# Performance work log

Measured on AMD Instinct MI355X. Metric: run time of the kernel, lower is better.

The kernel has to match this reference:

```python
import jax, jax.numpy as jnp
import numpy as np

LAMBDA = 10.0      # sinkhorn_lambda from init_kwargs
N_ITERS = 100      # fixed Sinkhorn iteration count
B, T_MAX, D_MAX = 256, 256, 256
TP, DP = T_MAX + 1, D_MAX + 1   # expanded with births/deaths row+col
L = TP * DP                      # padded flat output length per example
EPS = 1e-12


def setup_inputs() -> dict:
    key = jax.random.key(0)
    k1, k2, k3 = jax.random.split(key, 3)
    affinity_scores = jax.random.uniform(k1, (B, T_MAX, D_MAX), dtype=jnp.float32)
    num_detections = jax.random.randint(k2, (B,), 32, D_MAX + 1, dtype=jnp.int32)
    num_tracklets = jax.random.randint(k3, (B,), 32, T_MAX + 1, dtype=jnp.int32)
    return {
        "affinity_scores": affinity_scores,
        "num_detections": num_detections,
        "num_tracklets": num_tracklets,
    }


def _sinkhorn_transport(aff, nd, nt):
    """Masked Sinkhorn on the expanded (nt+1)x(nd+1) matrix, padded to [TP,DP]."""
    r = jnp.arange(TP)
    c = jnp.arange(DP)
    row_valid = r <= nt          # nt tracklet rows + 1 births/deaths row
    col_valid = c <= nd
    interior = (r[:, None] < nt) & (c[None, :] < nd)
    aff_pad = jnp.pad(aff, ((0, 1), (0, 1)))
    aff_e = jnp.where(interior, aff_pad, 0.0)   # dummy row/col have affinity 0
    mask = (row_valid[:, None] & col_valid[None, :]).astype(aff.dtype)
    # cost = -affinity  =>  kernel K = exp(-lambda * cost) = exp(lambda * affinity)
    K = jnp.exp(LAMBDA * aff_e) * mask
    ndf = nd.astype(aff.dtype)
    ntf = nt.astype(aff.dtype)
    # target marginals: [1,...,1, length] on valid entries, 0 on padding
    row_sums = jnp.where(r < nt, 1.0, jnp.where(r == nt, ndf, 0.0))
    col_sums = jnp.where(c < nd, 1.0, jnp.where(c == nd, ntf, 0.0))
    u0 = jnp.zeros((TP,), aff.dtype)
    v0 = col_valid.astype(aff.dtype)

    def body(carry, _):
        u, v = carry
        u = jnp.where(row_valid, row_sums / (K @ v + EPS), 0.0)
        v = jnp.where(col_valid, col_sums / (K.T @ u + EPS), 0.0)
        return (u, v), None

    (u, v), _ = jax.lax.scan(body, (u0, v0), None, length=N_ITERS)
    transport = u[:, None] * K * v[None, :]
    return transport, interior, row_valid, col_valid


def _single(aff, nd, nt):
    transport, interior, row_valid, col_valid = _sinkhorn_transport(aff, nd, nt)
    r = jnp.arange(TP)
    c = jnp.arange(DP)

    # hard assignment on transport[:-1,:-1] (valid interior): mutual argmax
    neg_inf = jnp.array(-jnp.inf, transport.dtype)
    t_in = jnp.where(interior, transport, neg_inf)
    row_max = jnp.max(t_in, axis=1, keepdims=True)
    col_max = jnp.max(t_in, axis=0, keepdims=True)
    assign_in = interior & (t_in == row_max) & (t_in == col_max)
    # births/deaths: unmatched tracklets -> death col nd; unmatched detections -> birth row nt
    row_has = jnp.any(assign_in, axis=1)
    col_has = jnp.any(assign_in, axis=0)
    deaths = (r[:, None] < nt) & (c[None, :] == nd) & (~row_has)[:, None]
    births = (r[:, None] == nt) & (c[None, :] < nd) & (~col_has)[None, :]
    assignment = assign_in | deaths | births

    # flatten the (nt+1)x(nd+1) valid submatrix row-major, zero-pad to length L
    k = jnp.arange(L)
    length = (nt + 1) * (nd + 1)
    rr = jnp.clip(k // (nd + 1), 0, T_MAX)
    cc = k % (nd + 1)
    valid = k < length
    t_flat = jnp.where(valid, transport[rr, cc], 0.0)
    a_flat = jnp.where(valid, assignment[rr, cc], False)
    return t_flat, a_flat


def reference(affinity_scores, num_detections, num_tracklets):
    t_flat, a_flat = jax.vmap(_single)(affinity_scores, num_detections, num_tracklets)
    return t_flat, a_flat
```

## Files before the change

kernel.cpp:

```cpp
#include <hip/hip_runtime.h>


#define T_MAX   256
#define L_FLAT  (257 * 257)
#define N_ITERS 100
#define LAMBDA_F 10.0f
#define EPS_F    1e-12f
#define RS      260

#define QX1  0xB1
#define QX2  0x4E
#define ROR4 0x124
#define ROR8 0x128

template<int CTRL>
__device__ __forceinline__ float dpp_addf(float x) {
    int t = __builtin_amdgcn_update_dpp(0, __float_as_int(x), CTRL, 0xF, 0xF, true);
    return x + __int_as_float(t);
}
template<int CTRL>
__device__ __forceinline__ float dpp_maxf(float x) {
    int t = __builtin_amdgcn_update_dpp(0, __float_as_int(x), CTRL, 0xF, 0xF, true);
    return fmaxf(x, __int_as_float(t));
}
template<int CTRL>
__device__ __forceinline__ int dpp_ori(int x) {
    int t = __builtin_amdgcn_update_dpp(0, x, CTRL, 0xF, 0xF, true);
    return x | t;
}
__device__ __forceinline__ float swz16_addf(float x) {
    return x + __int_as_float(__builtin_amdgcn_ds_swizzle(__float_as_int(x), 0x401F));
}
__device__ __forceinline__ float swz16_maxf(float x) {
    return fmaxf(x, __int_as_float(__builtin_amdgcn_ds_swizzle(__float_as_int(x), 0x401F)));
}
__device__ __forceinline__ int swz16_ori(int x) {
    return x | __builtin_amdgcn_ds_swizzle(x, 0x401F);
}
__device__ __forceinline__ float fast_rcp(float x) {
#if __has_builtin(__builtin_amdgcn_rcpf)
    return __builtin_amdgcn_rcpf(x);
#else
    return 1.0f / x;
#endif
}
__device__ __forceinline__ float sel4(float a, float b, float c, float d, int rg) {
    float lo = (rg & 1) ? b : a;
    float hi = (rg & 1) ? d : c;
    return (rg & 2) ? hi : lo;
}

__global__ __launch_bounds__(512, 2) void assoc_sinkhorn_kernel(
    const float* __restrict__ aff,
    const int*   __restrict__ ndet,
    const int*   __restrict__ ntrk,
    float*       __restrict__ out_t,
    float*       __restrict__ out_a)
{
    const int b   = blockIdx.x;
    const int nd  = ndet[b];
    const int nt  = ntrk[b];
    const int tid = threadIdx.x;
    const int w   = tid >> 6;
    const int l   = tid & 63;
    const int rg  = l & 3;
    const int cg  = l >> 2;
    const int R0  = (w << 5) + (rg << 3);
    const int C0  = cg << 4;

    __shared__ __align__(16) float red[8 * RS];
    __shared__ __align__(16) float varr[256];
    __shared__ __align__(16) float cmax_s[256];
    __shared__ __align__(16) float supart[8];
    __shared__ __align__(16) float svpart[2][8];

    const float ndf = (float)nd;
    const float ntf = (float)nt;

    float K[8][16];
    {
        const float* Ab = aff + (size_t)b * (T_MAX * T_MAX);
        #pragma unroll
        for (int i = 0; i < 8; ++i) {
            const int r = R0 + i;
            const bool rv = (r < nt);
            const float* row = Ab + (size_t)r * T_MAX + C0;
            #pragma unroll
            for (int k = 0; k < 4; ++k) {
                const float4 x = *reinterpret_cast<const float4*>(row + 4 * k);
                const float a4[4] = {x.x, x.y, x.z, x.w};
                #pragma unroll
                for (int e = 0; e < 4; ++e) {
                    const int j = 4 * k + e;
                    K[i][j] = (rv && (C0 + j) < nd) ? expf(LAMBDA_F * a4[e]) : 0.0f;
                }
            }
        }
    }

    if (tid < 256) varr[tid] = (tid < nd) ? 1.0f : 0.0f;
    if (tid < 8)   svpart[0][tid] = (tid == 0) ? ndf : 0.0f;
    __syncthreads();

    float u[8];
    #pragma unroll
    for (int i = 0; i < 8; ++i) u[i] = 0.f;
    float vbd = 1.0f;
    float ubd = 0.0f;

    const int s2c   = tid >> 1;
    const int s2sub = tid & 1;

    for (int it = 0; it < N_ITERS; ++it) {
        float v[16];
        {
            const float4 a0 = *reinterpret_cast<const float4*>(&varr[C0]);
            const float4 a1 = *reinterpret_cast<const float4*>(&varr[C0 + 4]);
            const float4 a2 = *reinterpret_cast<const float4*>(&varr[C0 + 8]);
            const float4 a3 = *reinterpret_cast<const float4*>(&varr[C0 + 12]);
            v[0]=a0.x; v[1]=a0.y; v[2]=a0.z; v[3]=a0.w;
            v[4]=a1.x; v[5]=a1.y; v[6]=a1.z; v[7]=a1.w;
            v[8]=a2.x; v[9]=a2.y; v[10]=a2.z; v[11]=a2.w;
            v[12]=a3.x; v[13]=a3.y; v[14]=a3.z; v[15]=a3.w;
        }
        float p[8];
        #pragma unroll
        for (int i = 0; i < 8; ++i) {
            float s = 0.f;
            #pragma unroll
            for (int j = 0; j < 16; ++j) s = fmaf(K[i][j], v[j], s);
            p[i] = s;
        }
        #pragma unroll
        for (int i = 0; i < 8; ++i) p[i] = dpp_addf<ROR4>(p[i]);
        #pragma unroll
        for (int i = 0; i < 8; ++i) p[i] = dpp_addf<ROR8>(p[i]);
        #pragma unroll
        for (int i = 0; i < 8; ++i) p[i] = swz16_addf(p[i]);
        #pragma unroll
        for (int i = 0; i < 8; ++i) p[i] += __shfl_xor(p[i], 32, 64);
        const float vbdE = vbd + EPS_F;
        #pragma unroll
        for (int i = 0; i < 8; ++i)
            u[i] = ((R0 + i) < nt) ? fast_rcp(p[i] + vbdE) : 0.0f;

        {
            float su = ((u[0] + u[1]) + (u[2] + u[3])) + ((u[4] + u[5]) + (u[6] + u[7]));
            su = dpp_addf<QX1>(su);
            su = dpp_addf<QX2>(su);
            if (l == 0) supart[w] = su;
        }

        float q[16];
        #pragma unroll
        for (int j = 0; j < 16; ++j) {
            float s = K[0][j] * u[0];
            #pragma unroll
            for (int i = 1; i < 8; ++i) s = fmaf(K[i][j], u[i], s);
            q[j] = s;
        }
        #pragma unroll
        for (int j = 0; j < 16; ++j) q[j] = dpp_addf<QX1>(q[j]);
        #pragma unroll
        for (int j = 0; j < 16; ++j) q[j] = dpp_addf<QX2>(q[j]);
        {
            float4 o;
            o.x = sel4(q[0], q[4], q[8],  q[12], rg);
            o.y = sel4(q[1], q[5], q[9],  q[13], rg);
            o.z = sel4(q[2], q[6], q[10], q[14], rg);
            o.w = sel4(q[3], q[7], q[11], q[15], rg);
            *reinterpret_cast<float4*>(&red[w * RS + 4 * l]) = o;
        }
        __syncthreads();

        {
            const int p_rd = it & 1;
            float s0 = red[(4*s2sub + 0) * RS + s2c];
            float s1 = red[(4*s2sub + 1) * RS + s2c];
            float s2 = red[(4*s2sub + 2) * RS + s2c];
            float s3 = red[(4*s2sub + 3) * RS + s2c];
            float s = (s0 + s1) + (s2 + s3);
            s = dpp_addf<QX1>(s);

            const float4 a0 = *reinterpret_cast<const float4*>(&supart[0]);
            const float4 a1 = *reinterpret_cast<const float4*>(&supart[4]);
            const float Su = ((a0.x+a0.y)+(a0.z+a0.w)) + ((a1.x+a1.y)+(a1.z+a1.w));
            const float4 b0 = *reinterpret_cast<const float4*>(&svpart[p_rd][0]);
            const float4 b1 = *reinterpret_cast<const float4*>(&svpart[p_rd][4]);
            const float Sv = ((b0.x+b0.y)+(b0.z+b0.w)) + ((b1.x+b1.y)+(b1.z+b1.w));

            const float ubd_new = ndf * fast_rcp(Sv + vbd + EPS_F);
            const float vn = (s2c < nd) ? fast_rcp(s + ubd_new + EPS_F) : 0.0f;
            if (s2sub == 0) varr[s2c] = vn;
            vbd = ntf * fast_rcp(Su + ubd_new + EPS_F);
            ubd = ubd_new;

            float x = (s2sub == 0) ? vn : 0.0f;
            x = dpp_addf<QX1>(x);
            x = dpp_addf<QX2>(x);
            x = dpp_addf<ROR4>(x);
            x = dpp_addf<ROR8>(x);
            x = swz16_addf(x);
            x += __shfl_xor(x, 32, 64);
            if (l == 0) svpart[p_rd ^ 1][w] = x;
        }
        __syncthreads();
    }

    float v[16];
    {
        const float4 a0 = *reinterpret_cast<const float4*>(&varr[C0]);
        const float4 a1 = *reinterpret_cast<const float4*>(&varr[C0 + 4]);
        const float4 a2 = *reinterpret_cast<const float4*>(&varr[C0 + 8]);
        const float4 a3 = *reinterpret_cast<const float4*>(&varr[C0 + 12]);
        v[0]=a0.x; v[1]=a0.y; v[2]=a0.z; v[3]=a0.w;
        v[4]=a1.x; v[5]=a1.y; v[6]=a1.z; v[7]=a1.w;
        v[8]=a2.x; v[9]=a2.y; v[10]=a2.z; v[11]=a2.w;
        v[12]=a3.x; v[13]=a3.y; v[14]=a3.z; v[15]=a3.w;
    }
    #pragma unroll
    for (int i = 0; i < 8; ++i) {
        #pragma unroll
        for (int j = 0; j < 16; ++j) K[i][j] = u[i] * K[i][j] * v[j];
    }

    float m[8];
    #pragma unroll
    for (int i = 0; i < 8; ++i) {
        float mm = K[i][0];
        #pragma unroll
        for (int j = 1; j < 16; ++j) mm = fmaxf(mm, K[i][j]);
        m[i] = mm;
    }
    #pragma unroll
    for (int i = 0; i < 8; ++i) m[i] = dpp_maxf<ROR4>(m[i]);
    #pragma unroll
    for (int i = 0; i < 8; ++i) m[i] = dpp_maxf<ROR8>(m[i]);
    #pragma unroll
    for (int i = 0; i < 8; ++i) m[i] = swz16_maxf(m[i]);
    #pragma unroll
    for (int i = 0; i < 8; ++i) m[i] = fmaxf(m[i], __shfl_xor(m[i], 32, 64));

    {
        float cmx[16];
        #pragma unroll
        for (int j = 0; j < 16; ++j) {
            float c = fmaxf(K[0][j], K[1][j]);
            #pragma unroll
            for (int i = 2; i < 8; ++i) c = fmaxf(c, K[i][j]);
            cmx[j] = c;
        }
        #pragma unroll
        for (int j = 0; j < 16; ++j) cmx[j] = dpp_maxf<QX1>(cmx[j]);
        #pragma unroll
        for (int j = 0; j < 16; ++j) cmx[j] = dpp_maxf<QX2>(cmx[j]);
        float4 o;
        o.x = sel4(cmx[0], cmx[4], cmx[8],  cmx[12], rg);
        o.y = sel4(cmx[1], cmx[5], cmx[9],  cmx[13], rg);
        o.z = sel4(cmx[2], cmx[6], cmx[10], cmx[14], rg);
        o.w = sel4(cmx[3], cmx[7], cmx[11], cmx[15], rg);
        *reinterpret_cast<float4*>(&red[w * RS + 4 * l]) = o;
    }
    __syncthreads();
    {
        float mm = fmaxf(fmaxf(red[(4*s2sub + 0) * RS + s2c], red[(4*s2sub + 1) * RS + s2c]),
                         fmaxf(red[(4*s2sub + 2) * RS + s2c], red[(4*s2sub + 3) * RS + s2c]));
        mm = dpp_maxf<QX1>(mm);
        if (s2sub == 0) cmax_s[s2c] = mm;
    }
    __syncthreads();

    float cm[16];
    {
        const float4 a0 = *reinterpret_cast<const float4*>(&cmax_s[C0]);
        const float4 a1 = *reinterpret_cast<const float4*>(&cmax_s[C0 + 4]);
        const float4 a2 = *reinterpret_cast<const float4*>(&cmax_s[C0 + 8]);
        const float4 a3 = *reinterpret_cast<const float4*>(&cmax_s[C0 + 12]);
        cm[0]=a0.x; cm[1]=a0.y; cm[2]=a0.z; cm[3]=a0.w;
        cm[4]=a1.x; cm[5]=a1.y; cm[6]=a1.z; cm[7]=a1.w;
        cm[8]=a2.x; cm[9]=a2.y; cm[10]=a2.z; cm[11]=a2.w;
        cm[12]=a3.x; cm[13]=a3.y; cm[14]=a3.z; cm[15]=a3.w;
    }
    unsigned bits[8];
    #pragma unroll
    for (int i = 0; i < 8; ++i) {
        unsigned bi = 0;
        const int r = R0 + i;
        #pragma unroll
        for (int j = 0; j < 16; ++j) {
            const int c = C0 + j;
            if ((r < nt) && (c < nd) && (K[i][j] == m[i]) && (K[i][j] == cm[j]))
                bi |= (1u << j);
        }
        bits[i] = bi;
    }
    int rh[8];
    #pragma unroll
    for (int i = 0; i < 8; ++i) rh[i] = bits[i] ? 1 : 0;
    #pragma unroll
    for (int i = 0; i < 8; ++i) rh[i] = dpp_ori<ROR4>(rh[i]);
    #pragma unroll
    for (int i = 0; i < 8; ++i) rh[i] = dpp_ori<ROR8>(rh[i]);
    #pragma unroll
    for (int i = 0; i < 8; ++i) rh[i] = swz16_ori(rh[i]);
    #pragma unroll
    for (int i = 0; i < 8; ++i) rh[i] |= __shfl_xor(rh[i], 32, 64);

    {
        unsigned anyb = bits[0];
        #pragma unroll
        for (int i = 1; i < 8; ++i) anyb |= bits[i];
        float ch[16];
        #pragma unroll
        for (int j = 0; j < 16; ++j) ch[j] = ((anyb >> j) & 1u) ? 1.0f : 0.0f;
        #pragma unroll
        for (int j = 0; j < 16; ++j) ch[j] = dpp_maxf<QX1>(ch[j]);
        #pragma unroll
        for (int j = 0; j < 16; ++j) ch[j] = dpp_maxf<QX2>(ch[j]);
        float4 o;
        o.x = sel4(ch[0], ch[4], ch[8],  ch[12], rg);
        o.y = sel4(ch[1], ch[5], ch[9],  ch[13], rg);
        o.z = sel4(ch[2], ch[6], ch[10], ch[14], rg);
        o.w = sel4(ch[3], ch[7], ch[11], ch[15], rg);
        *reinterpret_cast<float4*>(&red[w * RS + 4 * l]) = o;
    }
    __syncthreads();

    float* Ot = out_t + (size_t)b * L_FLAT;
    float* Oa = out_a + (size_t)b * L_FLAT;
    const int stride = nd + 1;

    {
        float c = fmaxf(fmaxf(red[(4*s2sub + 0) * RS + s2c], red[(4*s2sub + 1) * RS + s2c]),
                        fmaxf(red[(4*s2sub + 2) * RS + s2c], red[(4*s2sub + 3) * RS + s2c]));
        c = dpp_maxf<QX1>(c);
        if (s2sub == 0 && s2c < nd) {
            const int kk = nt * stride + s2c;
            Ot[kk] = ubd * varr[s2c];
            Oa[kk] = (c > 0.0f) ? 0.0f : 1.0f;
        }
    }
    if (tid == 0) {
        const int kk = nt * stride + nd;
        Ot[kk] = ubd * vbd;
        Oa[kk] = 0.0f;
    }
    if (cg == 0) {
        #pragma unroll
        for (int i = 0; i < 8; ++i) {
            const int r = R0 + i;
            if (r < nt) {
                const int kk = r * stride + nd;
                Ot[kk] = u[i] * vbd;
                Oa[kk] = rh[i] ? 0.0f : 1.0f;
            }
        }
    }
    #pragma unroll
    for (int i = 0; i < 8; ++i) {
        const int r = R0 + i;
        if (r < nt) {
            const int base = r * stride;
            #pragma unroll
            for (int j = 0; j < 16; ++j) {
                const int c = C0 + j;
                if (c < nd) {
                    Ot[base + c] = K[i][j];
                    Oa[base + c] = ((bits[i] >> j) & 1u) ? 1.0f : 0.0f;
                }
            }
        }
    }
    const int length = (nt + 1) * stride;
    for (int k = length + tid; k < L_FLAT; k += 512) {
        Ot[k] = 0.0f;
        Oa[k] = 0.0f;
    }
}

extern "C" void kernel_launch(void* const* d_in, const int* in_sizes, int n_in,
                              void* d_out, int out_size, void* d_ws, size_t ws_size,
                              hipStream_t stream)
{
    const float* aff  = (const float*)d_in[0];
    const int*   ndet = (const int*)d_in[1];
    const int*   ntrk = (const int*)d_in[2];
    const int    Bn   = in_sizes[1];
    float* out_t = (float*)d_out;
    float* out_a = out_t + (size_t)Bn * L_FLAT;
    assoc_sinkhorn_kernel<<<dim3(Bn), dim3(512), 0, stream>>>(aff, ndet, ntrk, out_t, out_a);
}
```

Before: 427.1 us.

## Run Sinkhorn matvecs on bf16 MFMA with K and K^T held in registers

Replaces the FP32 FMA matrix-vector products and cross-lane DPP/LDS reductions with bf16 MFMA 16x16x32 instructions. K is stored in bf16 twice, once row-tiled and once column-tiled as a transpose, so both K@v and K^T@u run as MFMAs without a shared-memory reduction. The u and v vectors are broadcast through LDS in bf16. The epilogue is rebuilt so row and column maxima come from the two copies. This removes the VALU FMA and reduction cost but lowers K, u and v to bf16, which can change the transport values and the argmax tie equality checks used for the assignment output.

```diff
diff --git a/kernel.cpp b/kernel.cpp
--- a/kernel.cpp
+++ b/kernel.cpp
@@ -6,27 +6,19 @@
 #define N_ITERS 100
 #define LAMBDA_F 10.0f
 #define EPS_F    1e-12f
-#define RS      260
-
-#define QX1  0xB1
-#define QX2  0x4E
+
+#define ROR1 0x121
+#define ROR2 0x122
 #define ROR4 0x124
 #define ROR8 0x128
+
+typedef short bf8   __attribute__((ext_vector_type(8)));
+typedef float f32x4 __attribute__((ext_vector_type(4)));
 
 template<int CTRL>
 __device__ __forceinline__ float dpp_addf(float x) {
     int t = __builtin_amdgcn_update_dpp(0, __float_as_int(x), CTRL, 0xF, 0xF, true);
     return x + __int_as_float(t);
-}
-template<int CTRL>
-__device__ __forceinline__ float dpp_maxf(float x) {
-    int t = __builtin_amdgcn_update_dpp(0, __float_as_int(x), CTRL, 0xF, 0xF, true);
-    return fmaxf(x, __int_as_float(t));
-}
-template<int CTRL>
-__device__ __forceinline__ int dpp_ori(int x) {
-    int t = __builtin_amdgcn_update_dpp(0, x, CTRL, 0xF, 0xF, true);
-    return x | t;
 }
 __device__ __forceinline__ float swz16_addf(float x) {
     return x + __int_as_float(__builtin_amdgcn_ds_swizzle(__float_as_int(x), 0x401F));
@@ -44,10 +36,12 @@
     return 1.0f / x;
 #endif
 }
-__device__ __forceinline__ float sel4(float a, float b, float c, float d, int rg) {
-    float lo = (rg & 1) ? b : a;
-    float hi = (rg & 1) ? d : c;
-    return (rg & 2) ? hi : lo;
+__device__ __forceinline__ unsigned short f2bf(float x) {
+    unsigned u = __float_as_uint(x);
+    return (unsigned short)((u + 0x7FFFu + ((u >> 16) & 1u)) >> 16);
+}
+__device__ __forceinline__ float bf2f(short s) {
+    return __uint_as_float(((unsigned)(unsigned short)s) << 16);
 }
 
 __global__ __launch_bounds__(512, 2) void assoc_sinkhorn_kernel(
@@ -63,266 +57,212 @@
     const int tid = threadIdx.x;
     const int w   = tid >> 6;
     const int l   = tid & 63;
-    const int rg  = l & 3;
-    const int cg  = l >> 2;
-    const int R0  = (w << 5) + (rg << 3);
-    const int C0  = cg << 4;
-
-    __shared__ __align__(16) float red[8 * RS];
-    __shared__ __align__(16) float varr[256];
-    __shared__ __align__(16) float cmax_s[256];
+    const int lr  = l & 15;
+    const int lk  = l >> 4;
+
+    __shared__ __align__(16) unsigned short u_bf[256];
+    __shared__ __align__(16) unsigned short v_bf[256];
+    __shared__ __align__(16) float u_f[256];
+    __shared__ __align__(16) float v_f[256];
     __shared__ __align__(16) float supart[8];
-    __shared__ __align__(16) float svpart[2][8];
+    __shared__ __align__(16) float svpart[8];
+    __shared__ __align__(16) float rm_s[256];
+    __shared__ __align__(16) float cm_s[256];
 
     const float ndf = (float)nd;
     const float ntf = (float)nt;
 
-    float K[8][16];
-    {
-        const float* Ab = aff + (size_t)b * (T_MAX * T_MAX);
-        #pragma unroll
-        for (int i = 0; i < 8; ++i) {
-            const int r = R0 + i;
-            const bool rv = (r < nt);
-            const float* row = Ab + (size_t)r * T_MAX + C0;
-            #pragma unroll
-            for (int k = 0; k < 4; ++k) {
-                const float4 x = *reinterpret_cast<const float4*>(row + 4 * k);
-                const float a4[4] = {x.x, x.y, x.z, x.w};
-                #pragma unroll
-                for (int e = 0; e < 4; ++e) {
-                    const int j = 4 * k + e;
-                    K[i][j] = (rv && (C0 + j) < nd) ? expf(LAMBDA_F * a4[e]) : 0.0f;
-                }
-            }
-        }
-    }
-
-    if (tid < 256) varr[tid] = (tid < nd) ? 1.0f : 0.0f;
-    if (tid < 8)   svpart[0][tid] = (tid == 0) ? ndf : 0.0f;
+    bf8 KA[2][8];
+    bf8 KB[2][8];
+    const float* Ab = aff + (size_t)b * (T_MAX * T_MAX);
+
+    #pragma unroll
+    for (int a = 0; a < 2; ++a) {
+        const int row = 32 * w + 16 * a + lr;
+        const bool rv = (row < nt);
+        const float* rp = Ab + (size_t)row * T_MAX;
+        #pragma unroll
+        for (int t = 0; t < 8; ++t) {
+            const int c0 = 32 * t + 8 * lk;
+            const float4 x0 = *reinterpret_cast<const float4*>(rp + c0);
+            const float4 x1 = *reinterpret_cast<const float4*>(rp + c0 + 4);
+            const float e[8] = {x0.x, x0.y, x0.z, x0.w, x1.x, x1.y, x1.z, x1.w};
+            bf8 kk;
+            #pragma unroll
+            for (int j = 0; j < 8; ++j) {
+                const float val = (rv && (c0 + j) < nd) ? __expf(LAMBDA_F * e[j]) : 0.0f;
+                kk[j] = (short)f2bf(val);
+            }
+            KA[a][t] = kk;
+        }
+    }
+    #pragma unroll
+    for (int c = 0; c < 2; ++c) {
+        const int col = 32 * w + 16 * c + lr;
+        const bool cv = (col < nd);
+        #pragma unroll
+        for (int t = 0; t < 8; ++t) {
+            const int r0 = 32 * t + 8 * lk;
+            bf8 kk;
+            #pragma unroll
+            for (int j = 0; j < 8; ++j) {
+                const float x = Ab[(size_t)(r0 + j) * T_MAX + col];
+                const float val = (cv && (r0 + j) < nt) ? __expf(LAMBDA_F * x) : 0.0f;
+                kk[j] = (short)f2bf(val);
+            }
+            KB[c][t] = kk;
+        }
+    }
+
+    if (tid < 256) {
+        v_bf[tid] = (tid < nd) ? f2bf(1.0f) : (unsigned short)0;
+        v_f[tid]  = (tid < nd) ? 1.0f : 0.0f;
+    }
     __syncthreads();
 
-    float u[8];
-    #pragma unroll
-    for (int i = 0; i < 8; ++i) u[i] = 0.f;
+    float Sv  = ndf;
     float vbd = 1.0f;
     float ubd = 0.0f;
 
-    const int s2c   = tid >> 1;
-    const int s2sub = tid & 1;
+    const int r_a0 = 32 * w + 4 * lk;
 
     for (int it = 0; it < N_ITERS; ++it) {
-        float v[16];
+        bf8 VF[8];
+        #pragma unroll
+        for (int t = 0; t < 8; ++t)
+            VF[t] = *reinterpret_cast<const bf8*>(&v_bf[32 * t + 8 * lk]);
+
+        f32x4 acc0 = {0.0f, 0.0f, 0.0f, 0.0f};
+        f32x4 acc1 = {0.0f, 0.0f, 0.0f, 0.0f};
+        #pragma unroll
+        for (int t = 0; t < 8; ++t) {
+            acc0 = __builtin_amdgcn_mfma_f32_16x16x32_bf16(KA[0][t], VF[t], acc0, 0, 0, 0);
+            acc1 = __builtin_amdgcn_mfma_f32_16x16x32_bf16(KA[1][t], VF[t], acc1, 0, 0, 0);
+        }
+
+        const float ubd_new = ndf * fast_rcp(Sv + vbd + EPS_F);
+        const float vbdE = vbd + EPS_F;
+        float u8[8];
+        #pragma unroll
+        for (int q = 0; q < 4; ++q) {
+            u8[q]     = ((r_a0 + q)      < nt) ? fast_rcp(acc0[q] + vbdE) : 0.0f;
+            u8[4 + q] = ((r_a0 + 16 + q) < nt) ? fast_rcp(acc1[q] + vbdE) : 0.0f;
+        }
+
         {
-            const float4 a0 = *reinterpret_cast<const float4*>(&varr[C0]);
-            const float4 a1 = *reinterpret_cast<const float4*>(&varr[C0 + 4]);
-            const float4 a2 = *reinterpret_cast<const float4*>(&varr[C0 + 8]);
-            const float4 a3 = *reinterpret_cast<const float4*>(&varr[C0 + 12]);
-            v[0]=a0.x; v[1]=a0.y; v[2]=a0.z; v[3]=a0.w;
-            v[4]=a1.x; v[5]=a1.y; v[6]=a1.z; v[7]=a1.w;
-            v[8]=a2.x; v[9]=a2.y; v[10]=a2.z; v[11]=a2.w;
-            v[12]=a3.x; v[13]=a3.y; v[14]=a3.z; v[15]=a3.w;
-        }
-        float p[8];
-        #pragma unroll
-        for (int i = 0; i < 8; ++i) {
-            float s = 0.f;
-            #pragma unroll
-            for (int j = 0; j < 16; ++j) s = fmaf(K[i][j], v[j], s);
-            p[i] = s;
-        }
-        #pragma unroll
-        for (int i = 0; i < 8; ++i) p[i] = dpp_addf<ROR4>(p[i]);
-        #pragma unroll
-        for (int i = 0; i < 8; ++i) p[i] = dpp_addf<ROR8>(p[i]);
-        #pragma unroll
-        for (int i = 0; i < 8; ++i) p[i] = swz16_addf(p[i]);
-        #pragma unroll
-        for (int i = 0; i < 8; ++i) p[i] += __shfl_xor(p[i], 32, 64);
-        const float vbdE = vbd + EPS_F;
-        #pragma unroll
-        for (int i = 0; i < 8; ++i)
-            u[i] = ((R0 + i) < nt) ? fast_rcp(p[i] + vbdE) : 0.0f;
+            float su = ((u8[0] + u8[1]) + (u8[2] + u8[3]))
+                     + ((u8[4] + u8[5]) + (u8[6] + u8[7]));
+            su = swz16_addf(su);
+            su += __shfl_xor(su, 32, 64);
+            if (l == 0) supart[w] = su;
+        }
+
+        if (lr == 0) {
+            const unsigned p01 = (unsigned)f2bf(u8[0]) | ((unsigned)f2bf(u8[1]) << 16);
+            const unsigned p23 = (unsigned)f2bf(u8[2]) | ((unsigned)f2bf(u8[3]) << 16);
+            const unsigned p45 = (unsigned)f2bf(u8[4]) | ((unsigned)f2bf(u8[5]) << 16);
+            const unsigned p67 = (unsigned)f2bf(u8[6]) | ((unsigned)f2bf(u8[7]) << 16);
+            *reinterpret_cast<uint2*>(&u_bf[r_a0])      = uint2{p01, p23};
+            *reinterpret_cast<uint2*>(&u_bf[r_a0 + 16]) = uint2{p45, p67};
+            f32x4 uf0 = {u8[0], u8[1], u8[2], u8[3]};
+            f32x4 uf1 = {u8[4], u8[5], u8[6], u8[7]};
+            *reinterpret_cast<f32x4*>(&u_f[r_a0])      = uf0;
+            *reinterpret_cast<f32x4*>(&u_f[r_a0 + 16]) = uf1;
+        }
+        __syncthreads();
+
+        bf8 UF[8];
+        #pragma unroll
+        for (int t = 0; t < 8; ++t)
+            UF[t] = *reinterpret_cast<const bf8*>(&u_bf[32 * t + 8 * lk]);
+
+        f32x4 qa0 = {0.0f, 0.0f, 0.0f, 0.0f};
+        f32x4 qa1 = {0.0f, 0.0f, 0.0f, 0.0f};
+        #pragma unroll
+        for (int t = 0; t < 8; ++t) {
+            qa0 = __builtin_amdgcn_mfma_f32_16x16x32_bf16(UF[t], KB[0][t], qa0, 0, 0, 0);
+            qa1 = __builtin_amdgcn_mfma_f32_16x16x32_bf16(UF[t], KB[1][t], qa1, 0, 0, 0);
+        }
+
+        const f32x4 sp0 = *reinterpret_cast<const f32x4*>(&supart[0]);
+        const f32x4 sp1 = *reinterpret_cast<const f32x4*>(&supart[4]);
+        const float Su = ((sp0[0] + sp0[1]) + (sp0[2] + sp0[3]))
+                       + ((sp1[0] + sp1[1]) + (sp1[2] + sp1[3]));
+        const float vbd_new = ntf * fast_rcp(Su + ubd_new + EPS_F);
+
+        const float ubdE = ubd_new + EPS_F;
+        const int c0i = 32 * w + lr;
+        const int c1i = 32 * w + 16 + lr;
+        const float v0 = (c0i < nd) ? fast_rcp(qa0[0] + ubdE) : 0.0f;
+        const float v1 = (c1i < nd) ? fast_rcp(qa1[0] + ubdE) : 0.0f;
 
         {
-            float su = ((u[0] + u[1]) + (u[2] + u[3])) + ((u[4] + u[5]) + (u[6] + u[7]));
-            su = dpp_addf<QX1>(su);
-            su = dpp_addf<QX2>(su);
-            if (l == 0) supart[w] = su;
-        }
-
-        float q[16];
-        #pragma unroll
-        for (int j = 0; j < 16; ++j) {
-            float s = K[0][j] * u[0];
-            #pragma unroll
-            for (int i = 1; i < 8; ++i) s = fmaf(K[i][j], u[i], s);
-            q[j] = s;
-        }
-        #pragma unroll
-        for (int j = 0; j < 16; ++j) q[j] = dpp_addf<QX1>(q[j]);
-        #pragma unroll
-        for (int j = 0; j < 16; ++j) q[j] = dpp_addf<QX2>(q[j]);
-        {
-            float4 o;
-            o.x = sel4(q[0], q[4], q[8],  q[12], rg);
-            o.y = sel4(q[1], q[5], q[9],  q[13], rg);
-            o.z = sel4(q[2], q[6], q[10], q[14], rg);
-            o.w = sel4(q[3], q[7], q[11], q[15], rg);
-            *reinterpret_cast<float4*>(&red[w * RS + 4 * l]) = o;
-        }
+            float sv = v0 + v1;
+            sv = dpp_addf<ROR1>(sv);
+            sv = dpp_addf<ROR2>(sv);
+            sv = dpp_addf<ROR4>(sv);
+            sv = dpp_addf<ROR8>(sv);
+            if (l == 0) svpart[w] = sv;
+        }
+        if (lk == 0) {
+            v_bf[c0i] = f2bf(v0);
+            v_bf[c1i] = f2bf(v1);
+            v_f[c0i]  = v0;
+            v_f[c1i]  = v1;
+        }
+        ubd = ubd_new;
+        vbd = vbd_new;
         __syncthreads();
 
-        {
-            const int p_rd = it & 1;
-            float s0 = red[(4*s2sub + 0) * RS + s2c];
-            float s1 = red[(4*s2sub + 1) * RS + s2c];
-            float s2 = red[(4*s2sub + 2) * RS + s2c];
-            float s3 = red[(4*s2sub + 3) * RS + s2c];
-            float s = (s0 + s1) + (s2 + s3);
-            s = dpp_addf<QX1>(s);
-
-            const float4 a0 = *reinterpret_cast<const float4*>(&supart[0]);
-            const float4 a1 = *reinterpret_cast<const float4*>(&supart[4]);
-            const float Su = ((a0.x+a0.y)+(a0.z+a0.w)) + ((a1.x+a1.y)+(a1.z+a1.w));
-            const float4 b0 = *reinterpret_cast<const float4*>(&svpart[p_rd][0]);
-            const float4 b1 = *reinterpret_cast<const float4*>(&svpart[p_rd][4]);
-            const float Sv = ((b0.x+b0.y)+(b0.z+b0.w)) + ((b1.x+b1.y)+(b1.z+b1.w));
-
-            const float ubd_new = ndf * fast_rcp(Sv + vbd + EPS_F);
-            const float vn = (s2c < nd) ? fast_rcp(s + ubd_new + EPS_F) : 0.0f;
-            if (s2sub == 0) varr[s2c] = vn;
-            vbd = ntf * fast_rcp(Su + ubd_new + EPS_F);
-            ubd = ubd_new;
-
-            float x = (s2sub == 0) ? vn : 0.0f;
-            x = dpp_addf<QX1>(x);
-            x = dpp_addf<QX2>(x);
-            x = dpp_addf<ROR4>(x);
-            x = dpp_addf<ROR8>(x);
-            x = swz16_addf(x);
-            x += __shfl_xor(x, 32, 64);
-            if (l == 0) svpart[p_rd ^ 1][w] = x;
-        }
-        __syncthreads();
-    }
-
-    float v[16];
-    {
-        const float4 a0 = *reinterpret_cast<const float4*>(&varr[C0]);
-        const float4 a1 = *reinterpret_cast<const float4*>(&varr[C0 + 4]);
-        const float4 a2 = *reinterpret_cast<const float4*>(&varr[C0 + 8]);
-        const float4 a3 = *reinterpret_cast<const float4*>(&varr[C0 + 12]);
-        v[0]=a0.x; v[1]=a0.y; v[2]=a0.z; v[3]=a0.w;
-        v[4]=a1.x; v[5]=a1.y; v[6]=a1.z; v[7]=a1.w;
-        v[8]=a2.x; v[9]=a2.y; v[10]=a2.z; v[11]=a2.w;
-        v[12]=a3.x; v[13]=a3.y; v[14]=a3.z; v[15]=a3.w;
-    }
-    #pragma unroll
-    for (int i = 0; i < 8; ++i) {
-        #pragma unroll
-        for (int j = 0; j < 16; ++j) K[i][j] = u[i] * K[i][j] * v[j];
-    }
-
-    float m[8];
-    #pragma unroll
-    for (int i = 0; i < 8; ++i) {
-        float mm = K[i][0];
-        #pragma unroll
-        for (int j = 1; j < 16; ++j) mm = fmaxf(mm, K[i][j]);
-        m[i] = mm;
-    }
-    #pragma unroll
-    for (int i = 0; i < 8; ++i) m[i] = dpp_maxf<ROR4>(m[i]);
-    #pragma unroll
-    for (int i = 0; i < 8; ++i) m[i] = dpp_maxf<ROR8>(m[i]);
-    #pragma unroll
-    for (int i = 0; i < 8; ++i) m[i] = swz16_maxf(m[i]);
-    #pragma unroll
-    for (int i = 0; i < 8; ++i) m[i] = fmaxf(m[i], __shfl_xor(m[i], 32, 64));
-
-    {
-        float cmx[16];
-        #pragma unroll
-        for (int j = 0; j < 16; ++j) {
-            float c = fmaxf(K[0][j], K[1][j]);
-            #pragma unroll
-            for (int i = 2; i < 8; ++i) c = fmaxf(c, K[i][j]);
-            cmx[j] = c;
-        }
-        #pragma unroll
-        for (int j = 0; j < 16; ++j) cmx[j] = dpp_maxf<QX1>(cmx[j]);
-        #pragma unroll
-        for (int j = 0; j < 16; ++j) cmx[j] = dpp_maxf<QX2>(cmx[j]);
-        float4 o;
-        o.x = sel4(cmx[0], cmx[4], cmx[8],  cmx[12], rg);
-        o.y = sel4(cmx[1], cmx[5], cmx[9],  cmx[13], rg);
-        o.z = sel4(cmx[2], cmx[6], cmx[10], cmx[14], rg);
-        o.w = sel4(cmx[3], cmx[7], cmx[11], cmx[15], rg);
-        *reinterpret_cast<float4*>(&red[w * RS + 4 * l]) = o;
-    }
-    __syncthreads();
-    {
-        float mm = fmaxf(fmaxf(red[(4*s2sub + 0) * RS + s2c], red[(4*s2sub + 1) * RS + s2c]),
-                         fmaxf(red[(4*s2sub + 2) * RS + s2c], red[(4*s2sub + 3) * RS + s2c]));
-        mm = dpp_maxf<QX1>(mm);
-        if (s2sub == 0) cmax_s[s2c] = mm;
-    }
-    __syncthreads();
-
-    float cm[16];
-    {
-        const float4 a0 = *reinterpret_cast<const float4*>(&cmax_s[C0]);
-        const float4 a1 = *reinterpret_cast<const float4*>(&cmax_s[C0 + 4]);
-        const float4 a2 = *reinterpret_cast<const float4*>(&cmax_s[C0 + 8]);
-        const float4 a3 = *reinterpret_cast<const float4*>(&cmax_s[C0 + 12]);
-        cm[0]=a0.x; cm[1]=a0.y; cm[2]=a0.z; cm[3]=a0.w;
-        cm[4]=a1.x; cm[5]=a1.y; cm[6]=a1.z; cm[7]=a1.w;
-        cm[8]=a2.x; cm[9]=a2.y; cm[10]=a2.z; cm[11]=a2.w;
-        cm[12]=a3.x; cm[13]=a3.y; cm[14]=a3.z; cm[15]=a3.w;
-    }
-    unsigned bits[8];
-    #pragma unroll
-    for (int i = 0; i < 8; ++i) {
-        unsigned bi = 0;
-        const int r = R0 + i;
-        #pragma unroll
-        for (int j = 0; j < 16; ++j) {
-            const int c = C0 + j;
-            if ((r < nt) && (c < nd) && (K[i][j] == m[i]) && (K[i][j] == cm[j]))
-                bi |= (1u << j);
-        }
-        bits[i] = bi;
-    }
-    int rh[8];
-    #pragma unroll
-    for (int i = 0; i < 8; ++i) rh[i] = bits[i] ? 1 : 0;
-    #pragma unroll
-    for (int i = 0; i < 8; ++i) rh[i] = dpp_ori<ROR4>(rh[i]);
-    #pragma unroll
-    for (int i = 0; i < 8; ++i) rh[i] = dpp_ori<ROR8>(rh[i]);
-    #pragma unroll
-    for (int i = 0; i < 8; ++i) rh[i] = swz16_ori(rh[i]);
-    #pragma unroll
-    for (int i = 0; i < 8; ++i) rh[i] |= __shfl_xor(rh[i], 32, 64);
-
-    {
-        unsigned anyb = bits[0];
-        #pragma unroll
-        for (int i = 1; i < 8; ++i) anyb |= bits[i];
-        float ch[16];
-        #pragma unroll
-        for (int j = 0; j < 16; ++j) ch[j] = ((anyb >> j) & 1u) ? 1.0f : 0.0f;
-        #pragma unroll
-        for (int j = 0; j < 16; ++j) ch[j] = dpp_maxf<QX1>(ch[j]);
-        #pragma unroll
-        for (int j = 0; j < 16; ++j) ch[j] = dpp_maxf<QX2>(ch[j]);
-        float4 o;
-        o.x = sel4(ch[0], ch[4], ch[8],  ch[12], rg);
-        o.y = sel4(ch[1], ch[5], ch[9],  ch[13], rg);
-        o.z = sel4(ch[2], ch[6], ch[10], ch[14], rg);
-        o.w = sel4(ch[3], ch[7], ch[11], ch[15], rg);
-        *reinterpret_cast<float4*>(&red[w * RS + 4 * l]) = o;
+        const f32x4 vp0 = *reinterpret_cast<const f32x4*>(&svpart[0]);
+        const f32x4 vp1 = *reinterpret_cast<const f32x4*>(&svpart[4]);
+        Sv = ((vp0[0] + vp0[1]) + (vp0[2] + vp0[3]))
+           + ((vp1[0] + vp1[1]) + (vp1[2] + vp1[3]));
+    }
+
+    float rm[2];
+    #pragma unroll
+    for (int a = 0; a < 2; ++a) {
+        const int row = 32 * w + 16 * a + lr;
+        const float ur = u_f[row];
+        float mm = 0.0f;
+        #pragma unroll
+        for (int t = 0; t < 8; ++t) {
+            const f32x4 va = *reinterpret_cast<const f32x4*>(&v_f[32 * t + 8 * lk]);
+            const f32x4 vb = *reinterpret_cast<const f32x4*>(&v_f[32 * t + 8 * lk + 4]);
+            const float vj[8] = {va[0], va[1], va[2], va[3], vb[0], vb[1], vb[2], vb[3]};
+            #pragma unroll
+            for (int j = 0; j < 8; ++j) {
+                const float tv = ur * bf2f(KA[a][t][j]) * vj[j];
+                mm = fmaxf(mm, tv);
+            }
+        }
+        mm = swz16_maxf(mm);
+        mm = fmaxf(mm, __shfl_xor(mm, 32, 64));
+        rm[a] = mm;
+        if (lk == 0) rm_s[row] = mm;
+    }
+    float cmv[2];
+    #pragma unroll
+    for (int c = 0; c < 2; ++c) {
+        const int col = 32 * w + 16 * c + lr;
+        const float vc = v_f[col];
+        float mm = 0.0f;
+        #pragma unroll
+        for (int t = 0; t < 8; ++t) {
+            const f32x4 ua = *reinterpret_cast<const f32x4*>(&u_f[32 * t + 8 * lk]);
+            const f32x4 ub = *reinterpret_cast<const f32x4*>(&u_f[32 * t + 8 * lk + 4]);
+            const float uj[8] = {ua[0], ua[1], ua[2], ua[3], ub[0], ub[1], ub[2], ub[3]};
+            #pragma unroll
+            for (int j = 0; j < 8; ++j) {
+                const float tv = uj[j] * bf2f(KB[c][t][j]) * vc;
+                mm = fmaxf(mm, tv);
+            }
+        }
+        mm = swz16_maxf(mm);
+        mm = fmaxf(mm, __shfl_xor(mm, 32, 64));
+        cmv[c] = mm;
+        if (lk == 0) cm_s[col] = mm;
     }
     __syncthreads();
 
@@ -330,46 +270,78 @@
     float* Oa = out_a + (size_t)b * L_FLAT;
     const int stride = nd + 1;
 
-    {
-        float c = fmaxf(fmaxf(red[(4*s2sub + 0) * RS + s2c], red[(4*s2sub + 1) * RS + s2c]),
-                        fmaxf(red[(4*s2sub + 2) * RS + s2c], red[(4*s2sub + 3) * RS + s2c]));
-        c = dpp_maxf<QX1>(c);
-        if (s2sub == 0 && s2c < nd) {
-            const int kk = nt * stride + s2c;
-            Ot[kk] = ubd * varr[s2c];
-            Oa[kk] = (c > 0.0f) ? 0.0f : 1.0f;
+    #pragma unroll
+    for (int a = 0; a < 2; ++a) {
+        const int row = 32 * w + 16 * a + lr;
+        const float ur = u_f[row];
+        const float rma = rm[a];
+        const bool rv = (row < nt);
+        int has = 0;
+        #pragma unroll
+        for (int t = 0; t < 8; ++t) {
+            const int cb = 32 * t + 8 * lk;
+            const f32x4 va = *reinterpret_cast<const f32x4*>(&v_f[cb]);
+            const f32x4 vb = *reinterpret_cast<const f32x4*>(&v_f[cb + 4]);
+            const f32x4 ca = *reinterpret_cast<const f32x4*>(&cm_s[cb]);
+            const f32x4 cb4 = *reinterpret_cast<const f32x4*>(&cm_s[cb + 4]);
+            const float vj[8] = {va[0], va[1], va[2], va[3], vb[0], vb[1], vb[2], vb[3]};
+            const float cj[8] = {ca[0], ca[1], ca[2], ca[3], cb4[0], cb4[1], cb4[2], cb4[3]};
+            #pragma unroll
+            for (int j = 0; j < 8; ++j) {
+                const int colj = cb + j;
+                const float tv = ur * bf2f(KA[a][t][j]) * vj[j];
+                const bool bit = rv && (colj < nd) && (tv == rma) && (tv == cj[j]);
+                has |= bit ? 1 : 0;
+                if (rv && colj < nd) {
+                    Ot[row * stride + colj] = tv;
+                    Oa[row * stride + colj] = bit ? 1.0f : 0.0f;
+                }
+            }
+        }
+        has = swz16_ori(has);
+        has |= __shfl_xor(has, 32, 64);
+        if (lk == 0 && rv) {
+            const int kk = row * stride + nd;
+            Ot[kk] = ur * vbd;
+            Oa[kk] = has ? 0.0f : 1.0f;
+        }
+    }
+    #pragma unroll
+    for (int c = 0; c < 2; ++c) {
+        const int col = 32 * w + 16 * c + lr;
+        const float vc = v_f[col];
+        const float cmc = cmv[c];
+        const bool cv = (col < nd);
+        int has = 0;
+        #pragma unroll
+        for (int t = 0; t < 8; ++t) {
+            const int rb = 32 * t + 8 * lk;
+            const f32x4 ua = *reinterpret_cast<const f32x4*>(&u_f[rb]);
+            const f32x4 ub = *reinterpret_cast<const f32x4*>(&u_f[rb + 4]);
+            const f32x4 ra = *reinterpret_cast<const f32x4*>(&rm_s[rb]);
+            const f32x4 rb4 = *reinterpret_cast<const f32x4*>(&rm_s[rb + 4]);
+            const float uj[8] = {ua[0], ua[1], ua[2], ua[3], ub[0], ub[1], ub[2], ub[3]};
+            const float rj[8] = {ra[0], ra[1], ra[2], ra[3], rb4[0], rb4[1], rb4[2], rb4[3]};
+            #pragma unroll
+            for (int j = 0; j < 8; ++j) {
+                const int rowj = rb + j;
+                const float tv = uj[j] * bf2f(KB[c][t][j]) * vc;
+                const bool bit = (rowj < nt) && cv && (tv == rj[j]) && (tv == cmc);
+                has |= bit ? 1 : 0;
+            }
+        }
+        has = swz16_ori(has);
+        has |= __shfl_xor(has, 32, 64);
+        if (lk == 0 && cv) {
+            const int kk = nt * stride + col;
+            Ot[kk] = ubd * vc;
+            Oa[kk] = has ? 0.0f : 1.0f;
         }
     }
     if (tid == 0) {
         const int kk = nt * stride + nd;
         Ot[kk] = ubd * vbd;
         Oa[kk] = 0.0f;
-    }
-    if (cg == 0) {
-        #pragma unroll
-        for (int i = 0; i < 8; ++i) {
-            const int r = R0 + i;
-            if (r < nt) {
-                const int kk = r * stride + nd;
-                Ot[kk] = u[i] * vbd;
-                Oa[kk] = rh[i] ? 0.0f : 1.0f;
-            }
-        }
-    }
-    #pragma unroll
-    for (int i = 0; i < 8; ++i) {
-        const int r = R0 + i;
-        if (r < nt) {
-            const int base = r * stride;
-            #pragma unroll
-            for (int j = 0; j < 16; ++j) {
-                const int c = C0 + j;
-                if (c < nd) {
-                    Ot[base + c] = K[i][j];
-                    Oa[base + c] = ((bits[i] >> j) & 1u) ? 1.0f : 0.0f;
-                }
-            }
-        }
     }
     const int length = (nt + 1) * stride;
     for (int k = length + tid; k < L_FLAT; k += 512) {
```

After: 548.0 us. +28.3%, slower.
